# Kernel optimization log

Measured on AMD Instinct MI355X. Metric: run time of the kernel, lower is better.

The kernel has to match this reference:

```python
import jax, jax.numpy as jnp
import numpy as np

NUM_NODES = 100000
NUM_EDGES = 1000000
NUM_REL = 3
NUM_GRAPHS = 512
VOCAB = 10000
EMBED_DIM = 64
HIDDEN_DIM = 64
NUM_CLS = 2


def setup_inputs() -> dict:
    key = jax.random.key(0)
    ks = jax.random.split(key, 10)
    x = jax.random.randint(ks[0], (NUM_NODES,), 0, VOCAB)
    edge_index = jax.random.randint(ks[1], (2, NUM_EDGES), 0, NUM_NODES)
    edge_type = jax.random.randint(ks[2], (NUM_EDGES,), 0, NUM_REL)
    batch = jnp.sort(jax.random.randint(ks[3], (NUM_NODES,), 0, NUM_GRAPHS))
    embed_table = jax.random.normal(ks[4], (VOCAB, EMBED_DIM), dtype=jnp.float32) * 0.02
    embed_table = embed_table.at[0].set(0.0)  # padding_idx=0
    W_rel = jax.random.normal(ks[5], (NUM_REL, EMBED_DIM, HIDDEN_DIM), dtype=jnp.float32) * 0.1
    W_root = jax.random.normal(ks[6], (EMBED_DIM, HIDDEN_DIM), dtype=jnp.float32) * 0.1
    conv_bias = jax.random.normal(ks[7], (HIDDEN_DIM,), dtype=jnp.float32) * 0.01
    lin_W = jax.random.normal(ks[8], (HIDDEN_DIM, NUM_CLS), dtype=jnp.float32) * 0.1
    lin_b = jnp.zeros((NUM_CLS,), dtype=jnp.float32)
    return {"x": x, "edge_index": edge_index, "edge_type": edge_type, "batch": batch,
            "embed_table": embed_table, "W_rel": W_rel, "W_root": W_root,
            "conv_bias": conv_bias, "lin_W": lin_W, "lin_b": lin_b}


def reference(x, edge_index, edge_type, batch, embed_table, W_rel, W_root, conv_bias, lin_W, lin_b):
    # Embedding lookup (padding row already zeroed)
    h = embed_table[x]                                   # [N, D]
    src, dst = edge_index[0], edge_index[1]
    # RGCNConv: root transform + per-relation mean-aggregated neighbor transform
    out = h @ W_root + conv_bias                          # [N, H]
    for r in range(NUM_REL):
        mask = (edge_type == r).astype(h.dtype)           # [E]
        hr = h @ W_rel[r]                                 # [N, H] tiny GEMM
        msg = hr[src] * mask[:, None]                     # [E, H] gather
        agg = jax.ops.segment_sum(msg, dst, num_segments=NUM_NODES)
        cnt = jax.ops.segment_sum(mask, dst, num_segments=NUM_NODES)
        out = out + agg / jnp.maximum(cnt, 1.0)[:, None]
    out = jax.nn.relu(out)
    # global_mean_pool over graph ids
    g_sum = jax.ops.segment_sum(out, batch, num_segments=NUM_GRAPHS)    # [G, H]
    g_cnt = jax.ops.segment_sum(jnp.ones_like(batch, dtype=out.dtype), batch, num_segments=NUM_GRAPHS)
    g_emb = g_sum / jnp.maximum(g_cnt, 1.0)[:, None]
    return g_emb @ lin_W + lin_b                          # [G, num_cls]
```

## Files before the change

kernel.cpp:

```cpp
#include <hip/hip_runtime.h>

#define N_NODES 100000
#define N_EDGES 1000000
#define N_GRAPHS 512
#define VOCAB 10000
#define DIM 64

#define NPB 64
#define NB 1563
#define EPB 4096
#define SB 245
#define NELEMS (NB * SB)
#define SCAN_B 1024
#define NSCAN ((NELEMS + SCAN_B - 1) / SCAN_B)
#define CAP 1152

typedef unsigned short ushort_t;

static __device__ __forceinline__ ushort_t f2bf(float f) {
    unsigned u = __float_as_uint(f);
    unsigned r = 0x7FFFu + ((u >> 16) & 1u);
    return (ushort_t)((u + r) >> 16);
}
#define BFLO(u) __uint_as_float((u) << 16)
#define BFHI(u) __uint_as_float((u) & 0xFFFF0000u)

__global__ void build_tables(const float* __restrict__ embed,
                             const float* __restrict__ W_rel,
                             const float* __restrict__ W_root,
                             ushort_t* __restrict__ Tb) {
    int tid  = blockIdx.x * 256 + threadIdx.x;
    int l    = tid & 63;
    int wave = tid >> 6;
    int sub  = l >> 4;
    int q    = l & 15;
    int row  = wave * 4 + sub;
    int m    = row / VOCAB;
    int v    = row - m * VOCAB;
    const float* W = (m == 0) ? W_root : (W_rel + (size_t)(m - 1) * DIM * DIM);
    float4 e4  = *(const float4*)(embed + (size_t)v * DIM + q * 4);
    float4 acc = {0.f, 0.f, 0.f, 0.f};
#pragma unroll
    for (int kk = 0; kk < 16; ++kk) {
        int srcl = sub * 16 + kk;
        float ex = __shfl(e4.x, srcl, 64);
        float ey = __shfl(e4.y, srcl, 64);
        float ez = __shfl(e4.z, srcl, 64);
        float ew = __shfl(e4.w, srcl, 64);
        const float4 w0 = *(const float4*)(W + (4 * kk + 0) * DIM + q * 4);
        const float4 w1 = *(const float4*)(W + (4 * kk + 1) * DIM + q * 4);
        const float4 w2 = *(const float4*)(W + (4 * kk + 2) * DIM + q * 4);
        const float4 w3 = *(const float4*)(W + (4 * kk + 3) * DIM + q * 4);
        acc.x += ex * w0.x; acc.y += ex * w0.y; acc.z += ex * w0.z; acc.w += ex * w0.w;
        acc.x += ey * w1.x; acc.y += ey * w1.y; acc.z += ey * w1.z; acc.w += ey * w1.w;
        acc.x += ez * w2.x; acc.y += ez * w2.y; acc.z += ez * w2.z; acc.w += ez * w2.w;
        acc.x += ew * w3.x; acc.y += ew * w3.y; acc.z += ew * w3.z; acc.w += ew * w3.w;
    }
    ushort_t* p = Tb + (size_t)row * DIM + q * 4;
    p[0] = f2bf(acc.x); p[1] = f2bf(acc.y);
    p[2] = f2bf(acc.z); p[3] = f2bf(acc.w);
}

__global__ __launch_bounds__(256)
void bucket_hist(const int* __restrict__ dst, int* __restrict__ bh,
                 float* __restrict__ g_sum) {
    for (int i = blockIdx.x * 256 + threadIdx.x; i < N_GRAPHS * DIM; i += SB * 256)
        g_sum[i] = 0.f;
    __shared__ int h[NB];
    for (int i = threadIdx.x; i < NB; i += 256) h[i] = 0;
    __syncthreads();
    int base = blockIdx.x * EPB;
    int lim  = base + EPB; if (lim > N_EDGES) lim = N_EDGES;
    for (int e = base + threadIdx.x; e < lim; e += 256)
        atomicAdd(&h[dst[e] >> 6], 1);
    __syncthreads();
    for (int i = threadIdx.x; i < NB; i += 256)
        bh[i * SB + blockIdx.x] = h[i];
}

__global__ __launch_bounds__(SCAN_B)
void scan_block(const int* __restrict__ bh, int* __restrict__ obh,
                int* __restrict__ bsum) {
    __shared__ int wsum[16];
    int i  = blockIdx.x * SCAN_B + threadIdx.x;
    int l  = threadIdx.x & 63;
    int wv = threadIdx.x >> 6;
    int v  = (i < NELEMS) ? bh[i] : 0;
    int s  = v;
#pragma unroll
    for (int d = 1; d < 64; d <<= 1) {
        int t = __shfl_up(s, d, 64);
        if (l >= d) s += t;
    }
    if (l == 63) wsum[wv] = s;
    __syncthreads();
    if (wv == 0) {
        int wval = (l < 16) ? wsum[l] : 0;
        int ss = wval;
#pragma unroll
        for (int d = 1; d < 16; d <<= 1) {
            int t = __shfl_up(ss, d, 64);
            if (l >= d) ss += t;
        }
        if (l == 15) bsum[blockIdx.x] = ss;
        if (l < 16)  wsum[l] = ss - wval;
    }
    __syncthreads();
    if (i < NELEMS) obh[i] = s - v + wsum[wv];
}

__global__ __launch_bounds__(SCAN_B)
void scan_add(int* __restrict__ obh, const int* __restrict__ bsum) {
    __shared__ int base_sh;
    int blk = blockIdx.x;
    if (threadIdx.x < 64) {
        int l = threadIdx.x;
        int t = 0;
        for (int i = l; i < blk; i += 64) t += bsum[i];
#pragma unroll
        for (int d = 32; d > 0; d >>= 1) t += __shfl_xor(t, d, 64);
        if (l == 0) base_sh = t;
    }
    __syncthreads();
    int i = blk * SCAN_B + threadIdx.x;
    if (i < NELEMS) obh[i] += base_sh;
}

__global__ __launch_bounds__(256)
void bucket_scatter(const int* __restrict__ src,
                    const int* __restrict__ dst,
                    const int* __restrict__ etype,
                    const int* __restrict__ x,
                    const int* __restrict__ obh,
                    unsigned* __restrict__ rec) {
    __shared__ int baseh[NB];
    __shared__ int h[NB];
    for (int i = threadIdx.x; i < NB; i += 256) {
        baseh[i] = obh[i * SB + blockIdx.x];
        h[i] = 0;
    }
    __syncthreads();
    int base = blockIdx.x * EPB;
    int lim  = base + EPB; if (lim > N_EDGES) lim = N_EDGES;
    for (int e = base + threadIdx.x; e < lim; e += 256) {
        int d = dst[e];
        int b = d >> 6;
        int rk = atomicAdd(&h[b], 1);
        unsigned payload = ((unsigned)x[src[e]] << 8)
                         | ((unsigned)(d & 63) << 2)
                         | (unsigned)etype[e];
        rec[baseh[b] + rk] = payload;
    }
}

__global__ __launch_bounds__(256)
void sort_aggregate(const int* __restrict__ x,
                    const int* __restrict__ batch,
                    const int* __restrict__ obh,
                    const unsigned* __restrict__ rec,
                    const ushort_t* __restrict__ Tb,
                    const float* __restrict__ bias,
                    float* __restrict__ g_sum) {
    __shared__ int cstart[257];
    __shared__ int cur[256];
    __shared__ int wsum4[4];
    __shared__ ushort_t sortedv[CAP];
    __shared__ float rows[NPB * DIM];
    __shared__ float red[256];
    __shared__ int batch_sh[NPB];
    int b = blockIdx.x, t = threadIdx.x;
    int s = obh[b * SB];
    int e = (b + 1 < NB) ? obh[(b + 1) * SB] : N_EDGES;
    int ne = e - s;
    int nvalid = N_NODES - b * NPB; if (nvalid > NPB) nvalid = NPB;

    cstart[t] = 0;
    if (t < NPB) batch_sh[t] = (t < nvalid) ? batch[b * NPB + t] : -1;
    __syncthreads();
    for (int i = t; i < ne; i += 256)
        atomicAdd(&cstart[rec[s + i] & 0xFFu], 1);
    __syncthreads();
    {
        int l = t & 63, wv = t >> 6;
        int v = cstart[t];
        int sc = v;
#pragma unroll
        for (int d = 1; d < 64; d <<= 1) {
            int tt = __shfl_up(sc, d, 64);
            if (l >= d) sc += tt;
        }
        if (l == 63) wsum4[wv] = sc;
        __syncthreads();
        if (t == 0) {
            int a = 0;
#pragma unroll
            for (int k = 0; k < 4; ++k) { int tmp = wsum4[k]; wsum4[k] = a; a += tmp; }
        }
        __syncthreads();
        int excl = sc - v + wsum4[wv];
        __syncthreads();
        cstart[t] = excl;
        cur[t] = excl;
        if (t == 255) cstart[256] = excl + v;
    }
    __syncthreads();
    for (int i = t; i < ne; i += 256) {
        unsigned p = rec[s + i];
        int rk = atomicAdd(&cur[p & 0xFFu], 1);
        sortedv[rk] = (ushort_t)(p >> 8);
    }
    __syncthreads();

    int grp = t >> 3;
    int sl  = t & 7;
#pragma unroll
    for (int nn = 0; nn < 2; ++nn) {
        int n = grp * 2 + nn;
        if (n >= nvalid) continue;
        int node = b * NPB + n;
        float a0 = 0.f, a1 = 0.f, a2 = 0.f, a3 = 0.f,
              a4 = 0.f, a5 = 0.f, a6 = 0.f, a7 = 0.f;
#pragma unroll
        for (int r = 0; r < 3; ++r) {
            int k  = (n << 2) | r;
            int s0 = cstart[k];
            int c  = cstart[k + 1] - s0;
            const ushort_t* tbase = Tb + (size_t)(1 + r) * VOCAB * DIM + sl * 8;
            float g0 = 0.f, g1 = 0.f, g2 = 0.f, g3 = 0.f,
                  g4 = 0.f, g5 = 0.f, g6 = 0.f, g7 = 0.f;
            for (int i = s0; i < s0 + c; ++i) {
                unsigned vv = sortedv[i];
                const uint4 tv = *(const uint4*)(tbase + (size_t)vv * DIM);
                g0 += BFLO(tv.x); g1 += BFHI(tv.x);
                g2 += BFLO(tv.y); g3 += BFHI(tv.y);
                g4 += BFLO(tv.z); g5 += BFHI(tv.z);
                g6 += BFLO(tv.w); g7 += BFHI(tv.w);
            }
            float iv = 1.f / fmaxf((float)c, 1.f);
            a0 += g0 * iv; a1 += g1 * iv; a2 += g2 * iv; a3 += g3 * iv;
            a4 += g4 * iv; a5 += g5 * iv; a6 += g6 * iv; a7 += g7 * iv;
        }
        int xv = x[node];
        const uint4 rt = *(const uint4*)(Tb + (size_t)xv * DIM + sl * 8);
        const float4 b0 = *(const float4*)(bias + sl * 8);
        const float4 b1 = *(const float4*)(bias + sl * 8 + 4);
        float* rp = rows + n * DIM + sl * 8;
        rp[0] = fmaxf(BFLO(rt.x) + b0.x + a0, 0.f);
        rp[1] = fmaxf(BFHI(rt.x) + b0.y + a1, 0.f);
        rp[2] = fmaxf(BFLO(rt.y) + b0.z + a2, 0.f);
        rp[3] = fmaxf(BFHI(rt.y) + b0.w + a3, 0.f);
        rp[4] = fmaxf(BFLO(rt.z) + b1.x + a4, 0.f);
        rp[5] = fmaxf(BFHI(rt.z) + b1.y + a5, 0.f);
        rp[6] = fmaxf(BFLO(rt.w) + b1.z + a6, 0.f);
        rp[7] = fmaxf(BFHI(rt.w) + b1.w + a7, 0.f);
    }
    __syncthreads();

    int gmin = batch_sh[0];
    int gmax = batch_sh[nvalid - 1];
    int f  = t & 63;
    int n0 = t >> 6;
    for (int g = gmin; g <= gmax; ++g) {
        float a = 0.f;
        for (int n = n0; n < nvalid; n += 4)
            a += (batch_sh[n] == g) ? rows[n * DIM + f] : 0.f;
        red[t] = a;
        __syncthreads();
        if (t < 64) {
            float tot = red[t] + red[t + 64] + red[t + 128] + red[t + 192];
            if (tot != 0.f) atomicAdd(&g_sum[g * DIM + t], tot);
        }
        __syncthreads();
    }
}

__device__ __forceinline__ int lbound(const int* __restrict__ b, int val) {
    int lo = 0, hi = N_NODES;
    while (lo < hi) {
        int mid = (lo + hi) >> 1;
        if (b[mid] < val) lo = mid + 1; else hi = mid;
    }
    return lo;
}

__global__ __launch_bounds__(64)
void final_linear(const int* __restrict__ batch,
                  const float* __restrict__ g_sum,
                  const float* __restrict__ lin_W,
                  const float* __restrict__ lin_b,
                  float* __restrict__ out) {
    int g = blockIdx.x;
    int l = threadIdx.x;
    int s = lbound(batch, g);
    int e = lbound(batch, g + 1);
    float mean = (e > s) ? g_sum[g * DIM + l] / (float)(e - s) : 0.f;
    float p0 = mean * lin_W[l * 2 + 0];
    float p1 = mean * lin_W[l * 2 + 1];
#pragma unroll
    for (int off2 = 32; off2 > 0; off2 >>= 1) {
        p0 += __shfl_down(p0, off2, 64);
        p1 += __shfl_down(p1, off2, 64);
    }
    if (l == 0) {
        out[g * 2 + 0] = p0 + lin_b[0];
        out[g * 2 + 1] = p1 + lin_b[1];
    }
}

extern "C" void kernel_launch(void* const* d_in, const int* in_sizes, int n_in,
                              void* d_out, int out_size, void* d_ws, size_t ws_size,
                              hipStream_t stream) {
    const int*   x      = (const int*)d_in[0];
    const int*   eidx   = (const int*)d_in[1];
    const int*   etype  = (const int*)d_in[2];
    const int*   batch  = (const int*)d_in[3];
    const float* embed  = (const float*)d_in[4];
    const float* W_rel  = (const float*)d_in[5];
    const float* W_root = (const float*)d_in[6];
    const float* bias   = (const float*)d_in[7];
    const float* lin_W  = (const float*)d_in[8];
    const float* lin_b  = (const float*)d_in[9];
    float* out = (float*)d_out;

    const int* src = eidx;
    const int* dst = eidx + N_EDGES;

    char* ws = (char*)d_ws;
    ushort_t* Tb    = (ushort_t*)(ws);
    unsigned* rec   = (unsigned*)(ws + 5120000);
    int* obh        = (int*)(ws + 9120000);
    int* bsum       = (int*)(ws + 10651776);
    int* bh         = (int*)(ws + 10653312);
    float* g_sum    = (float*)(ws + 12185088);

    bucket_hist<<<SB, 256, 0, stream>>>(dst, bh, g_sum);

    build_tables<<<(4 * VOCAB) / 16, 256, 0, stream>>>(embed, W_rel, W_root, Tb);

    scan_block<<<NSCAN, SCAN_B, 0, stream>>>(bh, obh, bsum);
    scan_add<<<NSCAN, SCAN_B, 0, stream>>>(obh, bsum);

    bucket_scatter<<<SB, 256, 0, stream>>>(src, dst, etype, x, obh, rec);

    sort_aggregate<<<NB, 256, 0, stream>>>(x, batch, obh, rec, Tb, bias, g_sum);

    final_linear<<<N_GRAPHS, 64, 0, stream>>>(batch, g_sum, lin_W, lin_b, out);
}
```

Measured before the change: 99.08 us.

## Fuse histogram with table build, restructure scan, flatten per-node aggregation loop

Merges the bucket histogram and the bf16 projection-table build into one launch so the two independent workloads share the grid. Replaces the flat two-pass scan with a per-bucket row scan plus a single-block scan over bucket totals, so the scatter and aggregate stages read bucket bases directly. Also raises the scatter block size to 512 threads. In the aggregation, full records are kept in LDS and all three relations for a node are walked in one loop, two edges per iteration, with a precomputed per-(node,relation) reciprocal count, which removes the per-relation inner-loop overhead. The extra per-edge LDS read of the reciprocal and the doubled sortedc footprint are added costs.

```diff
diff --git a/kernel.cpp b/kernel.cpp
--- a/kernel.cpp
+++ b/kernel.cpp
@@ -11,8 +11,7 @@
 #define EPB 4096
 #define SB 245
 #define NELEMS (NB * SB)
-#define SCAN_B 1024
-#define NSCAN ((NELEMS + SCAN_B - 1) / SCAN_B)
+#define BUILD_BLOCKS ((4 * VOCAB) / 16)
 #define CAP 1152
 
 typedef unsigned short ushort_t;
@@ -25,124 +24,137 @@
 #define BFLO(u) __uint_as_float((u) << 16)
 #define BFHI(u) __uint_as_float((u) & 0xFFFF0000u)
 
-__global__ void build_tables(const float* __restrict__ embed,
-                             const float* __restrict__ W_rel,
-                             const float* __restrict__ W_root,
-                             ushort_t* __restrict__ Tb) {
-    int tid  = blockIdx.x * 256 + threadIdx.x;
-    int l    = tid & 63;
-    int wave = tid >> 6;
-    int sub  = l >> 4;
-    int q    = l & 15;
-    int row  = wave * 4 + sub;
-    int m    = row / VOCAB;
-    int v    = row - m * VOCAB;
-    const float* W = (m == 0) ? W_root : (W_rel + (size_t)(m - 1) * DIM * DIM);
-    float4 e4  = *(const float4*)(embed + (size_t)v * DIM + q * 4);
-    float4 acc = {0.f, 0.f, 0.f, 0.f};
-#pragma unroll
-    for (int kk = 0; kk < 16; ++kk) {
-        int srcl = sub * 16 + kk;
-        float ex = __shfl(e4.x, srcl, 64);
-        float ey = __shfl(e4.y, srcl, 64);
-        float ez = __shfl(e4.z, srcl, 64);
-        float ew = __shfl(e4.w, srcl, 64);
-        const float4 w0 = *(const float4*)(W + (4 * kk + 0) * DIM + q * 4);
-        const float4 w1 = *(const float4*)(W + (4 * kk + 1) * DIM + q * 4);
-        const float4 w2 = *(const float4*)(W + (4 * kk + 2) * DIM + q * 4);
-        const float4 w3 = *(const float4*)(W + (4 * kk + 3) * DIM + q * 4);
-        acc.x += ex * w0.x; acc.y += ex * w0.y; acc.z += ex * w0.z; acc.w += ex * w0.w;
-        acc.x += ey * w1.x; acc.y += ey * w1.y; acc.z += ey * w1.z; acc.w += ey * w1.w;
-        acc.x += ez * w2.x; acc.y += ez * w2.y; acc.z += ez * w2.z; acc.w += ez * w2.w;
-        acc.x += ew * w3.x; acc.y += ew * w3.y; acc.z += ew * w3.z; acc.w += ew * w3.w;
-    }
-    ushort_t* p = Tb + (size_t)row * DIM + q * 4;
-    p[0] = f2bf(acc.x); p[1] = f2bf(acc.y);
-    p[2] = f2bf(acc.z); p[3] = f2bf(acc.w);
-}
-
 __global__ __launch_bounds__(256)
-void bucket_hist(const int* __restrict__ dst, int* __restrict__ bh,
-                 float* __restrict__ g_sum) {
-    for (int i = blockIdx.x * 256 + threadIdx.x; i < N_GRAPHS * DIM; i += SB * 256)
-        g_sum[i] = 0.f;
-    __shared__ int h[NB];
-    for (int i = threadIdx.x; i < NB; i += 256) h[i] = 0;
-    __syncthreads();
-    int base = blockIdx.x * EPB;
-    int lim  = base + EPB; if (lim > N_EDGES) lim = N_EDGES;
-    for (int e = base + threadIdx.x; e < lim; e += 256)
-        atomicAdd(&h[dst[e] >> 6], 1);
-    __syncthreads();
-    for (int i = threadIdx.x; i < NB; i += 256)
-        bh[i * SB + blockIdx.x] = h[i];
-}
-
-__global__ __launch_bounds__(SCAN_B)
-void scan_block(const int* __restrict__ bh, int* __restrict__ obh,
-                int* __restrict__ bsum) {
+void hist_build(const int* __restrict__ dst, int* __restrict__ bh,
+                float* __restrict__ g_sum,
+                const float* __restrict__ embed,
+                const float* __restrict__ W_rel,
+                const float* __restrict__ W_root,
+                ushort_t* __restrict__ Tb) {
+    if (blockIdx.x < SB) {
+        for (int i = blockIdx.x * 256 + threadIdx.x; i < N_GRAPHS * DIM; i += SB * 256)
+            g_sum[i] = 0.f;
+        __shared__ int h[NB];
+        for (int i = threadIdx.x; i < NB; i += 256) h[i] = 0;
+        __syncthreads();
+        int base = blockIdx.x * EPB;
+        int lim  = base + EPB; if (lim > N_EDGES) lim = N_EDGES;
+        for (int e = base + threadIdx.x; e < lim; e += 256)
+            atomicAdd(&h[dst[e] >> 6], 1);
+        __syncthreads();
+        for (int i = threadIdx.x; i < NB; i += 256)
+            bh[i * SB + blockIdx.x] = h[i];
+    } else {
+        int tid  = (blockIdx.x - SB) * 256 + threadIdx.x;
+        int l    = tid & 63;
+        int wave = tid >> 6;
+        int sub  = l >> 4;
+        int q    = l & 15;
+        int row  = wave * 4 + sub;
+        int m    = row / VOCAB;
+        int v    = row - m * VOCAB;
+        const float* W = (m == 0) ? W_root : (W_rel + (size_t)(m - 1) * DIM * DIM);
+        float4 e4  = *(const float4*)(embed + (size_t)v * DIM + q * 4);
+        float4 acc = {0.f, 0.f, 0.f, 0.f};
+#pragma unroll
+        for (int kk = 0; kk < 16; ++kk) {
+            int srcl = sub * 16 + kk;
+            float ex = __shfl(e4.x, srcl, 64);
+            float ey = __shfl(e4.y, srcl, 64);
+            float ez = __shfl(e4.z, srcl, 64);
+            float ew = __shfl(e4.w, srcl, 64);
+            const float4 w0 = *(const float4*)(W + (4 * kk + 0) * DIM + q * 4);
+            const float4 w1 = *(const float4*)(W + (4 * kk + 1) * DIM + q * 4);
+            const float4 w2 = *(const float4*)(W + (4 * kk + 2) * DIM + q * 4);
+            const float4 w3 = *(const float4*)(W + (4 * kk + 3) * DIM + q * 4);
+            acc.x += ex * w0.x; acc.y += ex * w0.y; acc.z += ex * w0.z; acc.w += ex * w0.w;
+            acc.x += ey * w1.x; acc.y += ey * w1.y; acc.z += ey * w1.z; acc.w += ey * w1.w;
+            acc.x += ez * w2.x; acc.y += ez * w2.y; acc.z += ez * w2.z; acc.w += ez * w2.w;
+            acc.x += ew * w3.x; acc.y += ew * w3.y; acc.z += ew * w3.z; acc.w += ew * w3.w;
+        }
+        ushort_t* p = Tb + (size_t)row * DIM + q * 4;
+        p[0] = f2bf(acc.x); p[1] = f2bf(acc.y);
+        p[2] = f2bf(acc.z); p[3] = f2bf(acc.w);
+    }
+}
+
+__global__ __launch_bounds__(256)
+void rowscan(const int* __restrict__ bh, int* __restrict__ loc,
+             int* __restrict__ btot) {
+    __shared__ int wsum4[4];
+    int b = blockIdx.x, t = threadIdx.x;
+    int l = t & 63, wv = t >> 6;
+    int v = (t < SB) ? bh[b * SB + t] : 0;
+    int sc = v;
+#pragma unroll
+    for (int d = 1; d < 64; d <<= 1) {
+        int tt = __shfl_up(sc, d, 64);
+        if (l >= d) sc += tt;
+    }
+    if (l == 63) wsum4[wv] = sc;
+    __syncthreads();
+    if (t == 0) {
+        int a = 0;
+#pragma unroll
+        for (int k = 0; k < 4; ++k) { int tmp = wsum4[k]; wsum4[k] = a; a += tmp; }
+    }
+    __syncthreads();
+    int excl = sc - v + wsum4[wv];
+    if (t < SB) loc[b * SB + t] = excl;
+    if (t == 255) btot[b] = excl;
+}
+
+__global__ __launch_bounds__(1024)
+void gscan(const int* __restrict__ btot, int* __restrict__ bbase) {
     __shared__ int wsum[16];
-    int i  = blockIdx.x * SCAN_B + threadIdx.x;
-    int l  = threadIdx.x & 63;
-    int wv = threadIdx.x >> 6;
-    int v  = (i < NELEMS) ? bh[i] : 0;
-    int s  = v;
+    int t = threadIdx.x;
+    int i0 = 2 * t, i1 = 2 * t + 1;
+    int a = (i0 < NB) ? btot[i0] : 0;
+    int c = (i1 < NB) ? btot[i1] : 0;
+    int pv = a + c;
+    int l = t & 63, wv = t >> 6;
+    int sc = pv;
 #pragma unroll
     for (int d = 1; d < 64; d <<= 1) {
-        int t = __shfl_up(s, d, 64);
-        if (l >= d) s += t;
-    }
-    if (l == 63) wsum[wv] = s;
+        int tt = __shfl_up(sc, d, 64);
+        if (l >= d) sc += tt;
+    }
+    if (l == 63) wsum[wv] = sc;
     __syncthreads();
     if (wv == 0) {
         int wval = (l < 16) ? wsum[l] : 0;
         int ss = wval;
 #pragma unroll
         for (int d = 1; d < 16; d <<= 1) {
-            int t = __shfl_up(ss, d, 64);
-            if (l >= d) ss += t;
-        }
-        if (l == 15) bsum[blockIdx.x] = ss;
-        if (l < 16)  wsum[l] = ss - wval;
-    }
-    __syncthreads();
-    if (i < NELEMS) obh[i] = s - v + wsum[wv];
-}
-
-__global__ __launch_bounds__(SCAN_B)
-void scan_add(int* __restrict__ obh, const int* __restrict__ bsum) {
-    __shared__ int base_sh;
-    int blk = blockIdx.x;
-    if (threadIdx.x < 64) {
-        int l = threadIdx.x;
-        int t = 0;
-        for (int i = l; i < blk; i += 64) t += bsum[i];
-#pragma unroll
-        for (int d = 32; d > 0; d >>= 1) t += __shfl_xor(t, d, 64);
-        if (l == 0) base_sh = t;
-    }
-    __syncthreads();
-    int i = blk * SCAN_B + threadIdx.x;
-    if (i < NELEMS) obh[i] += base_sh;
-}
-
-__global__ __launch_bounds__(256)
+            int tt = __shfl_up(ss, d, 64);
+            if (l >= d) ss += tt;
+        }
+        if (l < 16) wsum[l] = ss - wval;
+    }
+    __syncthreads();
+    int E = sc - pv + wsum[wv];
+    if (i0 <= NB) bbase[i0] = E;
+    if (i1 <= NB) bbase[i1] = E + a;
+}
+
+__global__ __launch_bounds__(512)
 void bucket_scatter(const int* __restrict__ src,
                     const int* __restrict__ dst,
                     const int* __restrict__ etype,
                     const int* __restrict__ x,
-                    const int* __restrict__ obh,
+                    const int* __restrict__ loc,
+                    const int* __restrict__ bbase,
                     unsigned* __restrict__ rec) {
     __shared__ int baseh[NB];
     __shared__ int h[NB];
-    for (int i = threadIdx.x; i < NB; i += 256) {
-        baseh[i] = obh[i * SB + blockIdx.x];
+    for (int i = threadIdx.x; i < NB; i += 512) {
+        baseh[i] = bbase[i] + loc[i * SB + blockIdx.x];
         h[i] = 0;
     }
     __syncthreads();
     int base = blockIdx.x * EPB;
     int lim  = base + EPB; if (lim > N_EDGES) lim = N_EDGES;
-    for (int e = base + threadIdx.x; e < lim; e += 256) {
+    for (int e = base + threadIdx.x; e < lim; e += 512) {
         int d = dst[e];
         int b = d >> 6;
         int rk = atomicAdd(&h[b], 1);
@@ -156,7 +168,7 @@
 __global__ __launch_bounds__(256)
 void sort_aggregate(const int* __restrict__ x,
                     const int* __restrict__ batch,
-                    const int* __restrict__ obh,
+                    const int* __restrict__ bbase,
                     const unsigned* __restrict__ rec,
                     const ushort_t* __restrict__ Tb,
                     const float* __restrict__ bias,
@@ -164,13 +176,14 @@
     __shared__ int cstart[257];
     __shared__ int cur[256];
     __shared__ int wsum4[4];
-    __shared__ ushort_t sortedv[CAP];
+    __shared__ float inv_sh[256];
+    __shared__ unsigned sortedc[CAP];
     __shared__ float rows[NPB * DIM];
     __shared__ float red[256];
     __shared__ int batch_sh[NPB];
     int b = blockIdx.x, t = threadIdx.x;
-    int s = obh[b * SB];
-    int e = (b + 1 < NB) ? obh[(b + 1) * SB] : N_EDGES;
+    int s = bbase[b];
+    int e = bbase[b + 1];
     int ne = e - s;
     int nvalid = N_NODES - b * NPB; if (nvalid > NPB) nvalid = NPB;
 
@@ -204,41 +217,53 @@
         if (t == 255) cstart[256] = excl + v;
     }
     __syncthreads();
+    inv_sh[t] = 1.f / fmaxf((float)(cstart[t + 1] - cstart[t]), 1.f);
     for (int i = t; i < ne; i += 256) {
         unsigned p = rec[s + i];
         int rk = atomicAdd(&cur[p & 0xFFu], 1);
-        sortedv[rk] = (ushort_t)(p >> 8);
+        sortedc[rk] = p;
     }
     __syncthreads();
 
     int grp = t >> 3;
     int sl  = t & 7;
+    const ushort_t* TbRel = Tb + (size_t)VOCAB * DIM;
 #pragma unroll
     for (int nn = 0; nn < 2; ++nn) {
         int n = grp * 2 + nn;
         if (n >= nvalid) continue;
         int node = b * NPB + n;
+        int i0 = cstart[n << 2];
+        int i1 = cstart[(n + 1) << 2];
         float a0 = 0.f, a1 = 0.f, a2 = 0.f, a3 = 0.f,
               a4 = 0.f, a5 = 0.f, a6 = 0.f, a7 = 0.f;
-#pragma unroll
-        for (int r = 0; r < 3; ++r) {
-            int k  = (n << 2) | r;
-            int s0 = cstart[k];
-            int c  = cstart[k + 1] - s0;
-            const ushort_t* tbase = Tb + (size_t)(1 + r) * VOCAB * DIM + sl * 8;
-            float g0 = 0.f, g1 = 0.f, g2 = 0.f, g3 = 0.f,
-                  g4 = 0.f, g5 = 0.f, g6 = 0.f, g7 = 0.f;
-            for (int i = s0; i < s0 + c; ++i) {
-                unsigned vv = sortedv[i];
-                const uint4 tv = *(const uint4*)(tbase + (size_t)vv * DIM);
-                g0 += BFLO(tv.x); g1 += BFHI(tv.x);
-                g2 += BFLO(tv.y); g3 += BFHI(tv.y);
-                g4 += BFLO(tv.z); g5 += BFHI(tv.z);
-                g6 += BFLO(tv.w); g7 += BFHI(tv.w);
-            }
-            float iv = 1.f / fmaxf((float)c, 1.f);
-            a0 += g0 * iv; a1 += g1 * iv; a2 += g2 * iv; a3 += g3 * iv;
-            a4 += g4 * iv; a5 += g5 * iv; a6 += g6 * iv; a7 += g7 * iv;
+        int i = i0;
+        for (; i + 2 <= i1; i += 2) {
+            unsigned c1 = sortedc[i], c2 = sortedc[i + 1];
+            const uint4 t1 = *(const uint4*)(TbRel +
+                ((size_t)(c1 & 3u) * VOCAB + (c1 >> 8)) * DIM + sl * 8);
+            const uint4 t2 = *(const uint4*)(TbRel +
+                ((size_t)(c2 & 3u) * VOCAB + (c2 >> 8)) * DIM + sl * 8);
+            float iv1 = inv_sh[c1 & 0xFFu];
+            float iv2 = inv_sh[c2 & 0xFFu];
+            a0 += BFLO(t1.x) * iv1; a1 += BFHI(t1.x) * iv1;
+            a2 += BFLO(t1.y) * iv1; a3 += BFHI(t1.y) * iv1;
+            a4 += BFLO(t1.z) * iv1; a5 += BFHI(t1.z) * iv1;
+            a6 += BFLO(t1.w) * iv1; a7 += BFHI(t1.w) * iv1;
+            a0 += BFLO(t2.x) * iv2; a1 += BFHI(t2.x) * iv2;
+            a2 += BFLO(t2.y) * iv2; a3 += BFHI(t2.y) * iv2;
+            a4 += BFLO(t2.z) * iv2; a5 += BFHI(t2.z) * iv2;
+            a6 += BFLO(t2.w) * iv2; a7 += BFHI(t2.w) * iv2;
+        }
+        if (i < i1) {
+            unsigned c1 = sortedc[i];
+            const uint4 t1 = *(const uint4*)(TbRel +
+                ((size_t)(c1 & 3u) * VOCAB + (c1 >> 8)) * DIM + sl * 8);
+            float iv1 = inv_sh[c1 & 0xFFu];
+            a0 += BFLO(t1.x) * iv1; a1 += BFHI(t1.x) * iv1;
+            a2 += BFLO(t1.y) * iv1; a3 += BFHI(t1.y) * iv1;
+            a4 += BFLO(t1.z) * iv1; a5 += BFHI(t1.z) * iv1;
+            a6 += BFLO(t1.w) * iv1; a7 += BFHI(t1.w) * iv1;
         }
         int xv = x[node];
         const uint4 rt = *(const uint4*)(Tb + (size_t)xv * DIM + sl * 8);
@@ -328,21 +353,22 @@
     char* ws = (char*)d_ws;
     ushort_t* Tb    = (ushort_t*)(ws);
     unsigned* rec   = (unsigned*)(ws + 5120000);
-    int* obh        = (int*)(ws + 9120000);
-    int* bsum       = (int*)(ws + 10651776);
-    int* bh         = (int*)(ws + 10653312);
-    float* g_sum    = (float*)(ws + 12185088);
-
-    bucket_hist<<<SB, 256, 0, stream>>>(dst, bh, g_sum);
-
-    build_tables<<<(4 * VOCAB) / 16, 256, 0, stream>>>(embed, W_rel, W_root, Tb);
-
-    scan_block<<<NSCAN, SCAN_B, 0, stream>>>(bh, obh, bsum);
-    scan_add<<<NSCAN, SCAN_B, 0, stream>>>(obh, bsum);
-
-    bucket_scatter<<<SB, 256, 0, stream>>>(src, dst, etype, x, obh, rec);
-
-    sort_aggregate<<<NB, 256, 0, stream>>>(x, batch, obh, rec, Tb, bias, g_sum);
+    int* loc        = (int*)(ws + 9120000);
+    int* btot       = (int*)(ws + 10651776);
+    int* bbase      = (int*)(ws + 10658048);
+    int* bh         = (int*)(ws + 10664320);
+    float* g_sum    = (float*)(ws + 12196096);
+
+    hist_build<<<SB + BUILD_BLOCKS, 256, 0, stream>>>(
+        dst, bh, g_sum, embed, W_rel, W_root, Tb);
+
+    rowscan<<<NB, 256, 0, stream>>>(bh, loc, btot);
+
+    gscan<<<1, 1024, 0, stream>>>(btot, bbase);
+
+    bucket_scatter<<<SB, 512, 0, stream>>>(src, dst, etype, x, loc, bbase, rec);
+
+    sort_aggregate<<<NB, 256, 0, stream>>>(x, batch, bbase, rec, Tb, bias, g_sum);
 
     final_linear<<<N_GRAPHS, 64, 0, stream>>>(batch, g_sum, lin_W, lin_b, out);
 }
```

New measurement: 87.46 us. 1.13x faster.
